# Performance work log

Measured on AMD Instinct MI355X. Metric: run time of the kernel, lower is better.

Reference implementation:

```python
import jax, jax.numpy as jnp
import numpy as np

NEG_INF = float('-inf')

def setup_inputs() -> dict:
    key = jax.random.key(0)
    k1, k2, k3, k4 = jax.random.split(key, 4)
    B, H, S, D = 2, 16, 2048, 64
    query = jax.random.normal(k1, (B, H, S, D), dtype=jnp.float32)
    k_ = jax.random.normal(k2, (B, H, S, D), dtype=jnp.float32)
    v_ = jax.random.normal(k3, (B, H, S, D), dtype=jnp.float32)
    attn_mask = jax.random.randint(k4, (B, S, S), 0, 2).astype(bool)
    # ensure diagonal is unmasked so every causal row has >=1 valid key
    diag = jnp.arange(S)
    attn_mask = attn_mask.at[:, diag, diag].set(True)
    return {"query": query, "key": k_, "value": v_, "attn_mask": attn_mask}

def reference(query, key, value, attn_mask):
    # query/key/value: [B, H, S, D]; attn_mask: [B, S, S] bool, True = keep
    B, H, S, D = query.shape
    scale = D ** (-0.5)
    scores = jnp.einsum('bhqd,bhkd->bhqk', query, key) * scale
    # custom mask (True = keep)
    scores = jnp.where(attn_mask[:, None, :, :], scores, NEG_INF)
    # causal mask: disallow j > i
    causal = jnp.triu(jnp.ones((S, S), dtype=bool), k=1)  # True above diagonal
    scores = jnp.where(causal[None, None, :, :], NEG_INF, scores)
    probs = jax.nn.softmax(scores, axis=-1)
    # dropout omitted (eval mode / deterministic reference)
    out = jnp.einsum('bhqk,bhkd->bhqd', probs, value)
    return out
```

## Files before the change

kernel.cpp:

```cpp
#include <hip/hip_runtime.h>
#include <hip/hip_bf16.h>

#define NS 2048
#define ND 64

typedef __attribute__((ext_vector_type(8))) short short8;
typedef __attribute__((ext_vector_type(4))) short short4v;
typedef __attribute__((ext_vector_type(4))) float f32x4;

static __device__ __forceinline__ short f2bf(float f) {
    union { __hip_bfloat16 h; short s; } u;
    u.h = __float2bfloat16(f);
    return u.s;
}
static __device__ __forceinline__ unsigned int pack2(float lo, float hi) {
    return (unsigned int)(unsigned short)f2bf(lo) |
           ((unsigned int)(unsigned short)f2bf(hi) << 16);
}
static __device__ __forceinline__ float exp2_fast(float x) {
    float r;
    asm("v_exp_f32 %0, %1" : "=v"(r) : "v"(x));
    return r;
}
static __device__ __forceinline__ unsigned int cvt_pk_bf16(float lo, float hi) {
    unsigned int w;
    asm("v_cvt_pk_bf16_f32 %0, %1, %2" : "=v"(w) : "v"(lo), "v"(hi));
    return w;
}

__global__ void detect_mask_kernel(const unsigned char* __restrict__ mask,
                                   int* __restrict__ flag) {
    const int i = threadIdx.x;
    unsigned int acc = 0;
    const uchar4* p = (const uchar4*)(mask + i * 64);
    #pragma unroll
    for (int j = 0; j < 16; ++j) {
        uchar4 v = p[j];
        acc |= (unsigned int)v.y | v.z | v.w;
    }
    const unsigned long long any = __ballot(acc != 0);
    if (i == 0) *flag = (any == 0ULL) ? 4 : 1;
}

__global__ void prep_all(const float* __restrict__ K,
                         const float* __restrict__ V,
                         const unsigned char* __restrict__ M,
                         const int* __restrict__ flag,
                         unsigned char* __restrict__ IMG,
                         unsigned int* __restrict__ Mbits) {
    if (blockIdx.x < 2048) {
        const int bid = blockIdx.x;
        const int bh = bid >> 6, T = bid & 63;
        const int i = threadIdx.x;
        __shared__ __align__(16) unsigned char img[8192];

        const int row = i >> 3;
        const int d0  = (i & 7) * 8;

        {
            const float* src = K + ((size_t)(bh * NS + T * 32 + row)) * ND + d0;
            float4 f0 = ((const float4*)src)[0];
            float4 f1 = ((const float4*)src)[1];
            const float f[8] = {f0.x, f0.y, f0.z, f0.w, f1.x, f1.y, f1.z, f1.w};
            const int n = row >> 4, cc = row & 15;
            #pragma unroll
            for (int jp = 0; jp < 4; ++jp) {
                const int d  = d0 + 2 * jp;
                const int ch = d >> 5, dd = d & 31;
                const int g  = (dd & 15) >> 2;
                const int jj = (dd >> 4) * 2 + ((dd >> 1) & 1);
                *(unsigned int*)(img + (n * 2 + ch) * 1024 + (g * 16 + cc) * 16 + jj * 4) =
                    pack2(f[2 * jp], f[2 * jp + 1]);
            }
        }
        {
            const int kv = row;
            const float* src = V + ((size_t)(bh * NS + T * 32 + kv)) * ND + d0;
            float4 f0 = ((const float4*)src)[0];
            float4 f1 = ((const float4*)src)[1];
            const float f[8] = {f0.x, f0.y, f0.z, f0.w, f1.x, f1.y, f1.z, f1.w};
            const int kl  = kv & ~1;
            const int q15 = kl & 15;
            const int g   = q15 >> 2;
            const int jj  = (kl >> 4) * 2 + ((q15 >> 1) & 1);
            const int half = (kv & 1) * 2;
            #pragma unroll
            for (int e = 0; e < 8; ++e) {
                const int d  = d0 + e;
                const int n4 = d >> 4, cv = d & 15;
                *(short*)(img + 4096 + n4 * 1024 + (g * 16 + cv) * 16 + jj * 4 + half) =
                    f2bf(f[e]);
            }
        }
        __syncthreads();
        uint4* dst = (uint4*)(IMG + ((size_t)bid << 13));
        const uint4* srcl = (const uint4*)img;
        dst[i * 2]     = srcl[i * 2];
        dst[i * 2 + 1] = srcl[i * 2 + 1];
    } else {
        const int id3 = (blockIdx.x - 2048) * 256 + threadIdx.x;
        const int tt = id3 & 63, q = (id3 >> 6) & 2047, b = id3 >> 17;
        const int ms = *flag;
        unsigned int w = 0;
        if (ms == 1) {
            const uint4* p = (const uint4*)(M + ((size_t)(b * NS + q)) * NS + tt * 32);
            uint4 A = p[0], B = p[1];
            const unsigned int u[8] = {A.x, A.y, A.z, A.w, B.x, B.y, B.z, B.w};
            #pragma unroll
            for (int i = 0; i < 8; ++i) {
                const unsigned int nib = (((u[i] & 0x01010101u) * 0x01020408u) >> 24) & 0xFu;
                w |= nib << (4 * i);
            }
        } else {
            const uint4* p = (const uint4*)(M + (((size_t)(b * NS + q)) * NS) * 4 + tt * 128);
            #pragma unroll
            for (int i = 0; i < 8; ++i) {
                uint4 A = p[i];
                w |= ((A.x & 1u) << (4 * i)) | ((A.y & 1u) << (4 * i + 1)) |
                     ((A.z & 1u) << (4 * i + 2)) | ((A.w & 1u) << (4 * i + 3));
            }
        }
        const int qrel = q - 32 * tt;
        if (qrel < 0) w = 0;
        else if (qrel < 31) w &= ((2u << qrel) - 1u);
        Mbits[((size_t)(b * 64 + (q >> 5)) * 64 + tt) * 32 + (q & 31)] = w;
    }
}

#define GLD(gsrc, ldst) __builtin_amdgcn_global_load_lds( \
    (const __attribute__((address_space(1))) unsigned int*)(gsrc), \
    (__attribute__((address_space(3))) unsigned int*)(ldst), 16, 0, 0)

__launch_bounds__(256, 4)
__global__ void attn_main(const float* __restrict__ Q,
                          const unsigned char* __restrict__ IMG,
                          const unsigned int* __restrict__ Mbits,
                          float* __restrict__ O) {
    const int idx = blockIdx.x;
    const int j   = (idx & 511) >> 5;
    const int bh  = idx & 31;
    const int qi  = (idx < 512) ? (31 - j) : j;
    const int b   = bh >> 4;

    const int tid  = threadIdx.x;
    const int wid  = tid >> 6;
    const int lane = tid & 63;
    const int g = lane >> 4;
    const int c = lane & 15;

    const int q0w = qi * 64 + wid * 16;

    const size_t bhoff = (size_t)bh * NS * ND;
    const float* Qb = Q + bhoff;
    float*       Ob = O + bhoff;
    const unsigned char* Tb = IMG + ((size_t)bh << 19);
    const unsigned int*  Mw = Mbits + ((size_t)(b * 64 + 2 * qi + (wid >> 1)) << 11);
    const int mko = ((wid & 1) << 4) + c;

    __shared__ __align__(16) unsigned char smem[2][16384];

    const float QS = 0.18033688f;
    short8 aq[2];
    {
        const float* qrow = Qb + (size_t)(q0w + c) * ND;
        #pragma unroll
        for (int ch = 0; ch < 2; ++ch) {
            float4 x0 = *reinterpret_cast<const float4*>(qrow + ch * 32 + g * 4);
            float4 x1 = *reinterpret_cast<const float4*>(qrow + ch * 32 + 16 + g * 4);
            short8 fr;
            fr[0]=f2bf(x0.x*QS); fr[1]=f2bf(x0.y*QS); fr[2]=f2bf(x0.z*QS); fr[3]=f2bf(x0.w*QS);
            fr[4]=f2bf(x1.x*QS); fr[5]=f2bf(x1.y*QS); fr[6]=f2bf(x1.z*QS); fr[7]=f2bf(x1.w*QS);
            aq[ch] = fr;
        }
    }

    const short ov = (c == 0) ? (short)0x3F80 : (short)0;
    short8 onesf;
    #pragma unroll
    for (int e = 0; e < 8; ++e) onesf[e] = ov;

    f32x4 acc[4];
    f32x4 acc_l = (f32x4){0.f, 0.f, 0.f, 0.f};
    #pragma unroll
    for (int n4 = 0; n4 < 4; ++n4) acc[n4] = (f32x4){0.f, 0.f, 0.f, 0.f};

    const int NP  = qi + 1;
    const int NTw = 2 * qi + (wid >> 1) + 1;

#define STAGE(B, TP) do { \
    const unsigned char* gp_ = Tb + ((size_t)(2 * (TP)) << 13) + (wid << 10) + (lane << 4); \
    unsigned char* lb_ = &smem[B][wid << 10]; \
    GLD(gp_,         lb_); \
    GLD(gp_ +  4096, lb_ +  4096); \
    GLD(gp_ +  8192, lb_ +  8192); \
    GLD(gp_ + 12288, lb_ + 12288); \
} while (0)

    STAGE(0, 0);
    unsigned int mk0 = Mw[mko];
    unsigned int mk1 = Mw[32 + mko];
    asm volatile("s_waitcnt vmcnt(0)" ::: "memory");
    __syncthreads();

    for (int tp = 0; tp < NP; ++tp) {
        const int cur = tp & 1;
        const bool havenext = (tp + 1 < NP);
        unsigned int nk0 = 0, nk1 = 0;
        if (havenext) {
            STAGE(cur ^ 1, tp + 1);
            nk0 = Mw[(2 * tp + 2) * 32 + mko];
            nk1 = Mw[(2 * tp + 3) * 32 + mko];
        }

        #pragma unroll
        for (int sub = 0; sub < 2; ++sub) {
            const int t = 2 * tp + sub;
            if (t < NTw) {
                const unsigned char* kb = smem[cur] + sub * 8192;
                const unsigned char* vb = kb + 4096;

                short8 kf[4], av[4];
                #pragma unroll
                for (int k4 = 0; k4 < 4; ++k4)
                    kf[k4] = *(const short8*)(kb + k4 * 1024 + (lane << 4));
                #pragma unroll
                for (int n4 = 0; n4 < 4; ++n4)
                    av[n4] = *(const short8*)(vb + n4 * 1024 + (lane << 4));

                f32x4 s0 = (f32x4){0.f, 0.f, 0.f, 0.f};
                f32x4 s1 = (f32x4){0.f, 0.f, 0.f, 0.f};
                s0 = __builtin_amdgcn_mfma_f32_16x16x32_bf16(kf[0], aq[0], s0, 0, 0, 0);
                s0 = __builtin_amdgcn_mfma_f32_16x16x32_bf16(kf[1], aq[1], s0, 0, 0, 0);
                s1 = __builtin_amdgcn_mfma_f32_16x16x32_bf16(kf[2], aq[0], s1, 0, 0, 0);
                s1 = __builtin_amdgcn_mfma_f32_16x16x32_bf16(kf[3], aq[1], s1, 0, 0, 0);

                const unsigned int mk = sub ? mk1 : mk0;

                float pv[8];
                #pragma unroll
                for (int r = 0; r < 4; ++r) {
                    const unsigned int b0 = (mk >> (4 * g + r)) & 1u;
                    const unsigned int b1 = (mk >> (16 + 4 * g + r)) & 1u;
                    pv[r]     = exp2_fast(b0 ? s0[r] : -INFINITY);
                    pv[4 + r] = exp2_fast(b1 ? s1[r] : -INFINITY);
                }
                union { unsigned int u[4]; short8 v; } pfu;
                pfu.u[0] = cvt_pk_bf16(pv[0], pv[1]);
                pfu.u[1] = cvt_pk_bf16(pv[2], pv[3]);
                pfu.u[2] = cvt_pk_bf16(pv[4], pv[5]);
                pfu.u[3] = cvt_pk_bf16(pv[6], pv[7]);
                const short8 pf = pfu.v;

                #pragma unroll
                for (int n4 = 0; n4 < 4; ++n4)
                    acc[n4] = __builtin_amdgcn_mfma_f32_16x16x32_bf16(av[n4], pf, acc[n4], 0, 0, 0);
                acc_l = __builtin_amdgcn_mfma_f32_16x16x32_bf16(onesf, pf, acc_l, 0, 0, 0);
            }
        }

        mk0 = nk0; mk1 = nk1;
        asm volatile("s_waitcnt vmcnt(0)" ::: "memory");
        __syncthreads();
    }

    {
        const int q = q0w + c;
        const float lsum = __shfl(acc_l[0], c);
        const float inv = (lsum > 0.f) ? (1.f / lsum) : 0.f;
        float* orow = Ob + (size_t)q * ND;
        #pragma unroll
        for (int n4 = 0; n4 < 4; ++n4) {
            float4 o;
            o.x = acc[n4][0] * inv;
            o.y = acc[n4][1] * inv;
            o.z = acc[n4][2] * inv;
            o.w = acc[n4][3] * inv;
            *(float4*)(orow + n4 * 16 + 4 * g) = o;
        }
    }
#undef STAGE
}

__launch_bounds__(128, 2)
__global__ void attn_fwd_fb(const float* __restrict__ Q,
                            const float* __restrict__ K,
                            const float* __restrict__ V,
                            const unsigned char* __restrict__ M,
                            float* __restrict__ O,
                            const int* __restrict__ mstride_p) {
    const int ms  = *mstride_p;
    const int idx = blockIdx.x;
    const int qi  = 31 - (idx >> 5);
    const int bh  = idx & 31;
    const int b   = bh >> 4;

    const int tid  = threadIdx.x;
    const int wid  = tid >> 6;
    const int lane = tid & 63;
    const int g = lane >> 4;
    const int c = lane & 15;

    const int q0w = qi * 64 + wid * 32;

    const size_t bhoff = (size_t)bh * NS * ND;
    const float* Qb = Q + bhoff;
    const float* Kb = K + bhoff;
    const float* Vb = V + bhoff;
    float*       Ob = O + bhoff;
    const unsigned char* Mb = M + (size_t)b * NS * NS * (size_t)ms;

    __shared__ __align__(16) unsigned char smem[2][8192];

    short8 aq[2][2];
    #pragma unroll
    for (int m = 0; m < 2; ++m) {
        const float* qrow = Qb + (size_t)(q0w + m * 16 + c) * ND;
        #pragma unroll
        for (int ch = 0; ch < 2; ++ch) {
            float4 x0 = *reinterpret_cast<const float4*>(qrow + ch * 32 + g * 4);
            float4 x1 = *reinterpret_cast<const float4*>(qrow + ch * 32 + 16 + g * 4);
            short8 fr;
            fr[0]=f2bf(x0.x); fr[1]=f2bf(x0.y); fr[2]=f2bf(x0.z); fr[3]=f2bf(x0.w);
            fr[4]=f2bf(x1.x); fr[5]=f2bf(x1.y); fr[6]=f2bf(x1.z); fr[7]=f2bf(x1.w);
            aq[m][ch] = fr;
        }
    }

    f32x4 acc[2][4];
    float m_run[2], l_run[2];
    #pragma unroll
    for (int m = 0; m < 2; ++m) {
        m_run[m] = -INFINITY; l_run[m] = 0.f;
        #pragma unroll
        for (int n4 = 0; n4 < 4; ++n4) acc[m][n4] = (f32x4){0.f, 0.f, 0.f, 0.f};
    }

    const int NT = 2 * qi + 2;

    const int krow = tid >> 2;
    const int kcb  = (tid & 3) * 16;
    const int ksw  = (krow & 7) << 4;
    const int vkp  = tid >> 3;
    const int vdb  = tid & 7;
    const int vg   = (vkp >> 1) & 3;
    const int vep  = (vkp & 1) + 2 * (vkp >> 3);
    const float* kbase = Kb + (size_t)krow * ND + kcb;
    const float* vbase = Vb + (size_t)(2 * vkp) * ND + vdb * 8;

    float4 kin0, kin1, kin2, kin3, vin0, vin1, vin2, vin3;

#define STAGE_LOAD(T) do { \
    const float* kp_ = kbase + (size_t)(T) * 32 * ND; \
    kin0 = *(const float4*)(kp_);      kin1 = *(const float4*)(kp_ + 4); \
    kin2 = *(const float4*)(kp_ + 8);  kin3 = *(const float4*)(kp_ + 12); \
    const float* vp_ = vbase + (size_t)(T) * 32 * ND; \
    vin0 = *(const float4*)(vp_);      vin1 = *(const float4*)(vp_ + 4); \
    vin2 = *(const float4*)(vp_ + ND); vin3 = *(const float4*)(vp_ + ND + 4); \
} while (0)

#define STAGE_WRITE(BUF) do { \
    unsigned char* kb_ = smem[BUF]; \
    short8 w0, w1; \
    w0[0]=f2bf(kin0.x); w0[1]=f2bf(kin0.y); w0[2]=f2bf(kin0.z); w0[3]=f2bf(kin0.w); \
    w0[4]=f2bf(kin1.x); w0[5]=f2bf(kin1.y); w0[6]=f2bf(kin1.z); w0[7]=f2bf(kin1.w); \
    w1[0]=f2bf(kin2.x); w1[1]=f2bf(kin2.y); w1[2]=f2bf(kin2.z); w1[3]=f2bf(kin2.w); \
    w1[4]=f2bf(kin3.x); w1[5]=f2bf(kin3.y); w1[6]=f2bf(kin3.z); w1[7]=f2bf(kin3.w); \
    *(short8*)(kb_ + krow * 128 + ((kcb * 2) ^ ksw))      = w0; \
    *(short8*)(kb_ + krow * 128 + ((kcb * 2 + 16) ^ ksw)) = w1; \
    unsigned char* vb_ = smem[BUF] + 4096; \
    const float lo_[8] = {vin0.x, vin0.y, vin0.z, vin0.w, vin1.x, vin1.y, vin1.z, vin1.w}; \
    const float hi_[8] = {vin2.x, vin2.y, vin2.z, vin2.w, vin3.x, vin3.y, vin3.z, vin3.w}; \
    _Pragma("unroll") \
    for (int j_ = 0; j_ < 8; ++j_) { \
        const int d_ = vdb * 8 + j_; \
        const int n4_ = d_ >> 4; \
        const int cc_ = d_ & 15; \
        const int aw_ = ((n4_ * 4 + vep) * 64 + ((vg * 16 + cc_) ^ ((vep << 3) | n4_))) * 4; \
        *(unsigned int*)(vb_ + aw_) = pack2(lo_[j_], hi_[j_]); \
    } \
} while (0)

    STAGE_LOAD(0);
    STAGE_WRITE(0);
    __syncthreads();

    const float SC = 0.125f;

    for (int t = 0; t < NT; ++t) {
        const int cur = t & 1;
        const bool havenext = (t + 1 < NT);
        if (havenext) STAGE_LOAD(t + 1);

        const unsigned char* kb = smem[cur];
        const int sw = (c & 7) << 4;
        short8 kf[2][2];
        #pragma unroll
        for (int n = 0; n < 2; ++n) {
            const int row = n * 16 + c;
            #pragma unroll
            for (int ch = 0; ch < 2; ++ch) {
                short4v lo = *(const short4v*)(kb + row * 128 + ((ch * 64 + g * 8) ^ sw));
                short4v hi = *(const short4v*)(kb + row * 128 + ((ch * 64 + g * 8 + 32) ^ sw));
                short8 fr;
                fr[0]=lo[0]; fr[1]=lo[1]; fr[2]=lo[2]; fr[3]=lo[3];
                fr[4]=hi[0]; fr[5]=hi[1]; fr[6]=hi[2]; fr[7]=hi[3];
                kf[n][ch] = fr;
            }
        }
        const unsigned char* vbuf = smem[cur] + 4096;
        short8 av[4];
        #pragma unroll
        for (int n4 = 0; n4 < 4; ++n4) {
            short8 fr;
            #pragma unroll
            for (int ep = 0; ep < 4; ++ep) {
                unsigned int w = *(const unsigned int*)
                    (vbuf + (((n4 * 4 + ep) * 64 + (lane ^ ((ep << 3) | n4))) * 4));
                fr[2 * ep]     = (short)(w & 0xffff);
                fr[2 * ep + 1] = (short)(w >> 16);
            }
            av[n4] = fr;
        }

        const int kv0 = t * 32;
        #pragma unroll
        for (int m = 0; m < 2; ++m) {
            const int q = q0w + m * 16 + c;

            f32x4 s[2];
            #pragma unroll
            for (int n = 0; n < 2; ++n) {
                f32x4 z = {0.f, 0.f, 0.f, 0.f};
                z = __builtin_amdgcn_mfma_f32_16x16x32_bf16(kf[n][0], aq[m][0], z, 0, 0, 0);
                z = __builtin_amdgcn_mfma_f32_16x16x32_bf16(kf[n][1], aq[m][1], z, 0, 0, 0);
                s[n] = z;
            }

            unsigned int mk0, mk1;
            if (ms == 1) {
                mk0 = *(const unsigned int*)(Mb + (size_t)q * NS + kv0 + 4 * g);
                mk1 = *(const unsigned int*)(Mb + (size_t)q * NS + kv0 + 16 + 4 * g);
            } else {
                const uint4 a4 = *(const uint4*)(Mb + ((size_t)q * NS + kv0 + 4 * g) * 4);
                const uint4 b4 = *(const uint4*)(Mb + ((size_t)q * NS + kv0 + 16 + 4 * g) * 4);
                mk0 = (a4.x?1u:0u) | (a4.y?0x100u:0u) | (a4.z?0x10000u:0u) | (a4.w?0x1000000u:0u);
                mk1 = (b4.x?1u:0u) | (b4.y?0x100u:0u) | (b4.z?0x10000u:0u) | (b4.w?0x1000000u:0u);
            }

            float mx = -INFINITY;
            #pragma unroll
            for (int n = 0; n < 2; ++n) {
                const unsigned int mk = n ? mk1 : mk0;
                #pragma unroll
                for (int r = 0; r < 4; ++r) {
                    const int kv = kv0 + n * 16 + 4 * g + r;
                    const bool keep = (((mk >> (8 * r)) & 0xffu) != 0u) && (kv <= q);
                    const float val = keep ? s[n][r] * SC : -INFINITY;
                    s[n][r] = val;
                    mx = fmaxf(mx, val);
                }
            }
            mx = fmaxf(mx, __shfl_xor(mx, 16));
            mx = fmaxf(mx, __shfl_xor(mx, 32));

            const float m_new = fmaxf(m_run[m], mx);
            const float alpha = (m_run[m] == -INFINITY) ? 0.f : __expf(m_run[m] - m_new);
            m_run[m] = m_new;
            const float msafe = (m_new == -INFINITY) ? 0.f : m_new;

            float sum = 0.f;
            short8 pf;
            #pragma unroll
            for (int n = 0; n < 2; ++n)
                #pragma unroll
                for (int r = 0; r < 4; ++r) {
                    const float pv = __expf(s[n][r] - msafe);
                    sum += pv;
                    pf[n * 4 + r] = f2bf(pv);
                }
            sum += __shfl_xor(sum, 16);
            sum += __shfl_xor(sum, 32);
            l_run[m] = l_run[m] * alpha + sum;

            #pragma unroll
            for (int n4 = 0; n4 < 4; ++n4) {
                f32x4 o = acc[m][n4];
                o[0] *= alpha; o[1] *= alpha; o[2] *= alpha; o[3] *= alpha;
                o = __builtin_amdgcn_mfma_f32_16x16x32_bf16(av[n4], pf, o, 0, 0, 0);
                acc[m][n4] = o;
            }
        }

        if (havenext) STAGE_WRITE(cur ^ 1);
        __syncthreads();
    }

    #pragma unroll
    for (int m = 0; m < 2; ++m) {
        const int q = q0w + m * 16 + c;
        const float inv = (l_run[m] > 0.f) ? (1.f / l_run[m]) : 0.f;
        float* orow = Ob + (size_t)q * ND;
        #pragma unroll
        for (int n4 = 0; n4 < 4; ++n4) {
            float4 o;
            o.x = acc[m][n4][0] * inv;
            o.y = acc[m][n4][1] * inv;
            o.z = acc[m][n4][2] * inv;
            o.w = acc[m][n4][3] * inv;
            *(float4*)(orow + n4 * 16 + 4 * g) = o;
        }
    }
#undef STAGE_LOAD
#undef STAGE_WRITE
}

extern "C" void kernel_launch(void* const* d_in, const int* in_sizes, int n_in,
                              void* d_out, int out_size, void* d_ws, size_t ws_size,
                              hipStream_t stream) {
    const float* Q = (const float*)d_in[0];
    const float* K = (const float*)d_in[1];
    const float* V = (const float*)d_in[2];
    const unsigned char* M = (const unsigned char*)d_in[3];
    float* O = (float*)d_out;

    unsigned char* ws = (unsigned char*)d_ws;
    int* flag = (int*)ws;
    const size_t IMG_SZ  = (size_t)2048 * 8192;
    const size_t BITS_SZ = (size_t)2 * 64 * 64 * 32 * 4;
    const size_t NEED = 1024 + IMG_SZ + BITS_SZ;

    hipLaunchKernelGGL(detect_mask_kernel, dim3(1), dim3(64), 0, stream, M, flag);

    if (ws_size >= NEED) {
        unsigned char* IMG  = ws + 1024;
        unsigned int* Mbits = (unsigned int*)(ws + 1024 + IMG_SZ);
        hipLaunchKernelGGL(prep_all, dim3(3072), dim3(256), 0, stream,
                           K, V, M, flag, IMG, Mbits);
        hipLaunchKernelGGL(attn_main, dim3(1024), dim3(256), 0, stream,
                           Q, IMG, Mbits, O);
    } else {
        hipLaunchKernelGGL(attn_fwd_fb, dim3(1024), dim3(128), 0, stream,
                           Q, K, V, M, O, flag);
    }
}
```

Measured before the change: 54.27 us.

## Split key tiles across wave pairs, each wave handling 32 query rows

The work split inside each block changes. Before, each wave owned 16 query rows and walked both 32-key sub-tiles of every staged pair. Now each wave owns 32 query rows (two 16-row MFMA groups) and handles only one sub-tile per pair, chosen by wave parity, so each K/V fragment read from LDS feeds twice as many MFMAs. The two partial accumulators, for output and row sums, are merged through shared memory at the end before normalisation. This costs more accumulator registers, an extra LDS reduction and barrier, and a parity-based imbalance on the causal diagonal.

```diff
diff --git a/kernel.cpp b/kernel.cpp
--- a/kernel.cpp
+++ b/kernel.cpp
@@ -147,22 +147,24 @@
     const int lane = tid & 63;
     const int g = lane >> 4;
     const int c = lane & 15;
-
-    const int q0w = qi * 64 + wid * 16;
+    const int p = wid & 1;
+    const int s = wid >> 1;
+
+    const int q0w = qi * 64 + s * 32;
 
     const size_t bhoff = (size_t)bh * NS * ND;
     const float* Qb = Q + bhoff;
     float*       Ob = O + bhoff;
     const unsigned char* Tb = IMG + ((size_t)bh << 19);
-    const unsigned int*  Mw = Mbits + ((size_t)(b * 64 + 2 * qi + (wid >> 1)) << 11);
-    const int mko = ((wid & 1) << 4) + c;
+    const unsigned int*  Mw = Mbits + ((size_t)(b * 64 + 2 * qi + s) << 11);
 
     __shared__ __align__(16) unsigned char smem[2][16384];
 
     const float QS = 0.18033688f;
-    short8 aq[2];
-    {
-        const float* qrow = Qb + (size_t)(q0w + c) * ND;
+    short8 aq[2][2];
+    #pragma unroll
+    for (int m = 0; m < 2; ++m) {
+        const float* qrow = Qb + (size_t)(q0w + m * 16 + c) * ND;
         #pragma unroll
         for (int ch = 0; ch < 2; ++ch) {
             float4 x0 = *reinterpret_cast<const float4*>(qrow + ch * 32 + g * 4);
@@ -170,7 +172,7 @@
             short8 fr;
             fr[0]=f2bf(x0.x*QS); fr[1]=f2bf(x0.y*QS); fr[2]=f2bf(x0.z*QS); fr[3]=f2bf(x0.w*QS);
             fr[4]=f2bf(x1.x*QS); fr[5]=f2bf(x1.y*QS); fr[6]=f2bf(x1.z*QS); fr[7]=f2bf(x1.w*QS);
-            aq[ch] = fr;
+            aq[m][ch] = fr;
         }
     }
 
@@ -179,13 +181,17 @@
     #pragma unroll
     for (int e = 0; e < 8; ++e) onesf[e] = ov;
 
-    f32x4 acc[4];
-    f32x4 acc_l = (f32x4){0.f, 0.f, 0.f, 0.f};
-    #pragma unroll
-    for (int n4 = 0; n4 < 4; ++n4) acc[n4] = (f32x4){0.f, 0.f, 0.f, 0.f};
-
-    const int NP  = qi + 1;
-    const int NTw = 2 * qi + (wid >> 1) + 1;
+    f32x4 acc[2][4];
+    f32x4 acc_l[2];
+    #pragma unroll
+    for (int m = 0; m < 2; ++m) {
+        acc_l[m] = (f32x4){0.f, 0.f, 0.f, 0.f};
+        #pragma unroll
+        for (int n4 = 0; n4 < 4; ++n4) acc[m][n4] = (f32x4){0.f, 0.f, 0.f, 0.f};
+    }
+
+    const int NP   = qi + 1;
+    const int tmax = 2 * qi + s;
 
 #define STAGE(B, TP) do { \
     const unsigned char* gp_ = Tb + ((size_t)(2 * (TP)) << 13) + (wid << 10) + (lane << 4); \
@@ -197,44 +203,44 @@
 } while (0)
 
     STAGE(0, 0);
-    unsigned int mk0 = Mw[mko];
-    unsigned int mk1 = Mw[32 + mko];
+    unsigned int mk0 = Mw[p * 32 + c];
+    unsigned int mk1 = Mw[p * 32 + 16 + c];
     asm volatile("s_waitcnt vmcnt(0)" ::: "memory");
     __syncthreads();
 
     for (int tp = 0; tp < NP; ++tp) {
         const int cur = tp & 1;
+        const int t = 2 * tp + p;
         const bool havenext = (tp + 1 < NP);
         unsigned int nk0 = 0, nk1 = 0;
         if (havenext) {
             STAGE(cur ^ 1, tp + 1);
-            nk0 = Mw[(2 * tp + 2) * 32 + mko];
-            nk1 = Mw[(2 * tp + 3) * 32 + mko];
-        }
-
-        #pragma unroll
-        for (int sub = 0; sub < 2; ++sub) {
-            const int t = 2 * tp + sub;
-            if (t < NTw) {
-                const unsigned char* kb = smem[cur] + sub * 8192;
-                const unsigned char* vb = kb + 4096;
-
-                short8 kf[4], av[4];
-                #pragma unroll
-                for (int k4 = 0; k4 < 4; ++k4)
-                    kf[k4] = *(const short8*)(kb + k4 * 1024 + (lane << 4));
-                #pragma unroll
-                for (int n4 = 0; n4 < 4; ++n4)
-                    av[n4] = *(const short8*)(vb + n4 * 1024 + (lane << 4));
-
+            nk0 = Mw[(t + 2) * 32 + c];
+            nk1 = Mw[(t + 2) * 32 + 16 + c];
+        }
+
+        if (t <= tmax) {
+            const unsigned char* kb = smem[cur] + (p << 13);
+            const unsigned char* vb = kb + 4096;
+
+            short8 kf[4], av[4];
+            #pragma unroll
+            for (int k4 = 0; k4 < 4; ++k4)
+                kf[k4] = *(const short8*)(kb + k4 * 1024 + (lane << 4));
+            #pragma unroll
+            for (int n4 = 0; n4 < 4; ++n4)
+                av[n4] = *(const short8*)(vb + n4 * 1024 + (lane << 4));
+
+            #pragma unroll
+            for (int m = 0; m < 2; ++m) {
                 f32x4 s0 = (f32x4){0.f, 0.f, 0.f, 0.f};
                 f32x4 s1 = (f32x4){0.f, 0.f, 0.f, 0.f};
-                s0 = __builtin_amdgcn_mfma_f32_16x16x32_bf16(kf[0], aq[0], s0, 0, 0, 0);
-                s0 = __builtin_amdgcn_mfma_f32_16x16x32_bf16(kf[1], aq[1], s0, 0, 0, 0);
-                s1 = __builtin_amdgcn_mfma_f32_16x16x32_bf16(kf[2], aq[0], s1, 0, 0, 0);
-                s1 = __builtin_amdgcn_mfma_f32_16x16x32_bf16(kf[3], aq[1], s1, 0, 0, 0);
-
-                const unsigned int mk = sub ? mk1 : mk0;
+                s0 = __builtin_amdgcn_mfma_f32_16x16x32_bf16(kf[0], aq[m][0], s0, 0, 0, 0);
+                s0 = __builtin_amdgcn_mfma_f32_16x16x32_bf16(kf[1], aq[m][1], s0, 0, 0, 0);
+                s1 = __builtin_amdgcn_mfma_f32_16x16x32_bf16(kf[2], aq[m][0], s1, 0, 0, 0);
+                s1 = __builtin_amdgcn_mfma_f32_16x16x32_bf16(kf[3], aq[m][1], s1, 0, 0, 0);
+
+                const unsigned int mk = m ? mk1 : mk0;
 
                 float pv[8];
                 #pragma unroll
@@ -253,8 +259,8 @@
 
                 #pragma unroll
                 for (int n4 = 0; n4 < 4; ++n4)
-                    acc[n4] = __builtin_amdgcn_mfma_f32_16x16x32_bf16(av[n4], pf, acc[n4], 0, 0, 0);
-                acc_l = __builtin_amdgcn_mfma_f32_16x16x32_bf16(onesf, pf, acc_l, 0, 0, 0);
+                    acc[m][n4] = __builtin_amdgcn_mfma_f32_16x16x32_bf16(av[n4], pf, acc[m][n4], 0, 0, 0);
+                acc_l[m] = __builtin_amdgcn_mfma_f32_16x16x32_bf16(onesf, pf, acc_l[m], 0, 0, 0);
             }
         }
 
@@ -263,19 +269,45 @@
         __syncthreads();
     }
 
-    {
-        const int q = q0w + c;
-        const float lsum = __shfl(acc_l[0], c);
-        const float inv = (lsum > 0.f) ? (1.f / lsum) : 0.f;
-        float* orow = Ob + (size_t)q * ND;
-        #pragma unroll
-        for (int n4 = 0; n4 < 4; ++n4) {
-            float4 o;
-            o.x = acc[n4][0] * inv;
-            o.y = acc[n4][1] * inv;
-            o.z = acc[n4][2] * inv;
-            o.w = acc[n4][3] * inv;
-            *(float4*)(orow + n4 * 16 + 4 * g) = o;
+    float* MB = (float*)smem;
+    __syncthreads();
+    if (p == 1) {
+        #pragma unroll
+        for (int m = 0; m < 2; ++m) {
+            #pragma unroll
+            for (int n4 = 0; n4 < 4; ++n4)
+                *(f32x4*)&MB[(((s * 2 + m) * 4 + n4) * 64 + lane) * 4] = acc[m][n4];
+            *(f32x4*)&MB[4096 + ((s * 2 + m) * 64 + lane) * 4] = acc_l[m];
+        }
+    }
+    __syncthreads();
+    if (p == 0) {
+        #pragma unroll
+        for (int m = 0; m < 2; ++m) {
+            #pragma unroll
+            for (int n4 = 0; n4 < 4; ++n4) {
+                f32x4 o = *(const f32x4*)&MB[(((s * 2 + m) * 4 + n4) * 64 + lane) * 4];
+                acc[m][n4][0] += o[0]; acc[m][n4][1] += o[1];
+                acc[m][n4][2] += o[2]; acc[m][n4][3] += o[3];
+            }
+            f32x4 ol = *(const f32x4*)&MB[4096 + ((s * 2 + m) * 64 + lane) * 4];
+            acc_l[m][0] += ol[0];
+        }
+        #pragma unroll
+        for (int m = 0; m < 2; ++m) {
+            const int q = q0w + m * 16 + c;
+            const float lsum = __shfl(acc_l[m][0], c);
+            const float inv = (lsum > 0.f) ? (1.f / lsum) : 0.f;
+            float* orow = Ob + (size_t)q * ND;
+            #pragma unroll
+            for (int n4 = 0; n4 < 4; ++n4) {
+                float4 o;
+                o.x = acc[m][n4][0] * inv;
+                o.y = acc[m][n4][1] * inv;
+                o.z = acc[m][n4][2] * inv;
+                o.w = acc[m][n4][3] * inv;
+                *(float4*)(orow + n4 * 16 + 4 * g) = o;
+            }
         }
     }
 #undef STAGE
@@ -474,9 +506,9 @@
             for (int n = 0; n < 2; ++n)
                 #pragma unroll
                 for (int r = 0; r < 4; ++r) {
-                    const float pv = __expf(s[n][r] - msafe);
-                    sum += pv;
-                    pf[n * 4 + r] = f2bf(pv);
+                    const float pvv = __expf(s[n][r] - msafe);
+                    sum += pvv;
+                    pf[n * 4 + r] = f2bf(pvv);
                 }
             sum += __shfl_xor(sum, 16);
             sum += __shfl_xor(sum, 32);
```

Result: no change. 54.28 us (+0.0%).
